# Performance work log

Hardware: AMD Instinct MI355X
Metric: run time of the kernel (lower is better)

Reference implementation:

```python
import jax, jax.numpy as jnp
import numpy as np

CANVAS = 512
SCORE_THR = 0.02
NMS_THR = 0.45
LVTOP = 1000      # cfg['lvtop'] for mm source
IMTOP = 200       # cfg['imtop']
NMS_PRE = 2000    # fixed pre-NMS candidate cap (static shape for jit)
NUM_CLASSES = 80
STRIDES = [8, 16, 32, 64, 128, 256, 512]
AR3 = [False, True, True, True, True, False, False]


def _make_priors():
    # get_scales(512): smallest=0.04, rmin=0.1, rmax=0.9, n=7
    smallest, rmin, rmax, n = 0.04, 0.1, 0.9, 7
    step = (rmax - rmin) / (n - 2)
    scales = [smallest] + [rmin + i * step for i in range(n)]
    sz = np.round(np.array(scales) * CANVAS).astype(np.int64)
    pr, lvlen = [], []
    for i, s in enumerate(STRIDES):
        fs = CANVAS // s
        ratios = [1.0, 2.0, 0.5] + ([3.0, 1.0 / 3.0] if AR3[i] else [])
        wh = [(sz[i] * np.sqrt(r), sz[i] / np.sqrt(r)) for r in ratios]
        extra = np.sqrt(float(sz[i]) * float(sz[i + 1]))  # sqrt(sz[i+1]/sz[i])*sz[i]
        wh.insert(1, (extra, extra))
        wh = np.array(wh, np.float32)            # [na, 2]
        xs = (np.arange(fs, dtype=np.float32) + 0.5) * s
        cx, cy = np.meshgrid(xs, xs)             # rows index y
        ctr = np.stack([cx, cy], -1)[:, :, None, :]  # [fs, fs, 1, 2]
        na = wh.shape[0]
        p = np.concatenate([np.broadcast_to(ctr, (fs, fs, na, 2)),
                            np.broadcast_to(wh, (fs, fs, na, 2))], -1).reshape(-1, 4)
        pr.append(p)
        lvlen.append(p.shape[0])
    return np.concatenate(pr).astype(np.float32), lvlen

PRIORS_NP, LVLEN = _make_priors()   # total 24564, lvlen=[16384,6144,1536,384,96,16,4]


def setup_inputs() -> dict:
    key = jax.random.key(0)
    k1, k2 = jax.random.split(key)
    A = PRIORS_NP.shape[0]
    cls_logits = jax.random.normal(k1, (4, A, NUM_CLASSES + 1), dtype=jnp.float32)
    reg = jax.random.normal(k2, (4, A, 4), dtype=jnp.float32)
    priors = jnp.asarray(PRIORS_NP)
    return {"cls_logits": cls_logits, "reg": reg, "priors": priors}


def _pairwise_iou(b):  # b: [K,4] xyxy
    area = (b[:, 2] - b[:, 0]) * (b[:, 3] - b[:, 1])
    lt = jnp.maximum(b[:, None, :2], b[None, :, :2])
    rb = jnp.minimum(b[:, None, 2:], b[None, :, 2:])
    wh = jnp.clip(rb - lt, 0.0)
    inter = wh[..., 0] * wh[..., 1]
    return inter / jnp.maximum(area[:, None] + area[None, :] - inter, 1e-6)


def _nms_keep(b):  # boxes sorted by descending score, class-offset applied
    m = _pairwise_iou(b) * jnp.triu(jnp.ones((NMS_PRE, NMS_PRE), b.dtype), 1)
    def body(sup, i):
        sup = sup | ((~sup[i]) & (m[i] > NMS_THR))
        return sup, None
    sup, _ = jax.lax.scan(body, jnp.zeros((NMS_PRE,), bool), jnp.arange(NMS_PRE))
    return ~sup


def reference(cls_logits, reg, priors):
    N = cls_logits.shape[0]
    C = NUM_CLASSES
    # softmax, background class is LAST (bckg_class_first=False for mm source)
    scr = jax.nn.softmax(cls_logits, axis=-1)[..., :-1]
    scr = jnp.where(scr > SCORE_THR, scr, 0.0)  # score threshold (fidx filter)
    # per-level top-k over flattened (anchor, class) pairs  [post.top_per_level]
    vals_l, anch_l, cls_l = [], [], []
    start = 0
    for lv in LVLEN:
        f = scr[:, start:start + lv, :].reshape(N, lv * C)
        k = min(LVTOP, lv * C)
        v, idx = jax.lax.top_k(f, k)
        vals_l.append(v)
        anch_l.append(start + idx // C)
        cls_l.append(idx % C)
        start += lv
    vals = jnp.concatenate(vals_l, 1)
    anch = jnp.concatenate(anch_l, 1)
    cls = jnp.concatenate(cls_l, 1)
    # fixed-size pre-NMS cap (static shapes under jit)
    v2, sel = jax.lax.top_k(vals, NMS_PRE)
    anch = jnp.take_along_axis(anch, sel, 1)
    cls = jnp.take_along_axis(cls, sel, 1)
    # decode boxes  [post.decode_boxes, mults=(0.1, 0.2), clamp=True]
    p = priors[anch]                                 # [N,K,4] cxcywh
    r = jnp.take_along_axis(reg, anch[..., None], 1)  # [N,K,4]
    cx = p[..., 0] + r[..., 0] * 0.1 * p[..., 2]
    cy = p[..., 1] + r[..., 1] * 0.1 * p[..., 3]
    w = p[..., 2] * jnp.exp(r[..., 2] * 0.2)
    h = p[..., 3] * jnp.exp(r[..., 3] * 0.2)
    boxes = jnp.stack([cx - w / 2, cy - h / 2, cx + w / 2, cy + h / 2], -1)
    boxes = jnp.clip(boxes, 0.0, float(CANVAS))
    # class-aware NMS via class offsets
    nb = boxes + cls.astype(boxes.dtype)[..., None] * (2.0 * CANVAS)
    keep = jax.vmap(_nms_keep)(nb)                   # [N,K] bool
    fs = jnp.where(keep & (v2 > 0), v2, 0.0)
    fv, fi = jax.lax.top_k(fs, IMTOP)                # imtop
    fb = jnp.take_along_axis(boxes, fi[..., None], 1)
    fc = jnp.take_along_axis(cls, fi, 1)
    fb = jnp.where(fv[..., None] > 0, fb, 0.0)
    return fb, fv, fc
```

## Files before the change

### kernel.cpp

```cpp
#include <hip/hip_runtime.h>
#include <hip/hip_bf16.h>
#include <math.h>

typedef unsigned long long u64;
typedef unsigned int u32;

#define A_TOTAL 24564
#define NCLS 80
#define NIMG 4
#define NPRE 2000
#define NLV 7
#define HBUCKETS 1024
#define BEXP_BASE 0x3CA3
#define TOTAL_G (NIMG * A_TOTAL)
#define FA 64
#define FT 256
#define NBLK_F ((TOTAL_G + FA - 1) / FA)
#define POOL_CAP_MAX 4096
#define CAPSEL 4608
#define MROWS 512
#define FTILES (MROWS / 16)

__device__ __constant__ int c_klv[NLV] = {1000,1000,1000,1000,1000,1000,320};

#define WS_HIST      0
#define WS_MCOUNT    114688
#define WS_BCOUNT    114800
#define WS_ZERO_END  114912
#define WS_PCOUNT    114912
#define WS_MAIN      121280
#define WS_BND       350656
#define WS_BOXES     1268160
#define WS_CLS       1396160
#define WS_SCORE     1428160
#define WS_MASK      1460160
#define WS_POOL      3508160

#define NZERO_W (WS_ZERO_END / 4)

__device__ inline u64 shfl_u64(u64 v, int src) {
  int lo = __shfl((int)(u32)(v & 0xFFFFFFFFULL), src);
  int hi = __shfl((int)(u32)(v >> 32), src);
  return ((u64)(u32)hi << 32) | (u32)lo;
}

__device__ inline int score_bucket(u32 bits) {
  int b = (int)(bits >> 16) - BEXP_BASE;
  return b < 0 ? 0 : (b > HBUCKETS - 1 ? HBUCKETS - 1 : b);
}

__device__ inline int level_of(int a) {
  return (a < 16384) ? 0 : (a < 22528) ? 1 : (a < 24064) ? 2 :
         (a < 24448) ? 3 : (a < 24544) ? 4 : (a < 24560) ? 5 : 6;
}

__global__ __launch_bounds__(256) void k_zero(u32* __restrict__ p) {
  int i = blockIdx.x * 256 + threadIdx.x;
  if (i < NZERO_W) p[i] = 0;
}

__device__ inline void score20(const float* __restrict__ logits, int g, int q,
                               float (&e)[20], float& rt) {
  const float* row = logits + (size_t)g * 81;
  float x[20];
#pragma unroll
  for (int i = 0; i < 20; ++i) x[i] = row[q * 20 + i];
  float x80 = (q == 3) ? row[80] : 0.f;
  float mloc = x[0];
#pragma unroll
  for (int i = 1; i < 20; ++i) mloc = fmaxf(mloc, x[i]);
  if (q == 3) mloc = fmaxf(mloc, x80);
  float m = fmaxf(mloc, __shfl_xor(mloc, 1));
  m = fmaxf(m, __shfl_xor(m, 2));
  float tq = 0.f;
#pragma unroll
  for (int i = 0; i < 20; ++i) { e[i] = expf(x[i] - m); tq += e[i]; }
  if (q == 3) tq += expf(x80 - m);
  float t = tq + __shfl_xor(tq, 1);
  t = t + __shfl_xor(t, 2);
  rt = 1.0f / t;
}

__device__ inline void wave_find_cut(const u32* __restrict__ h, int k, int lane,
                                     int& cx, int& cy) {
  u32 s = 0;
#pragma unroll
  for (int i = 0; i < 16; ++i) s += h[lane * 16 + i];
  u32 S = s;
#pragma unroll
  for (int o = 1; o < 64; o <<= 1) {
    u32 t = (u32)__shfl_down((int)S, o);
    if (lane + o < 64) S += t;
  }
  u32 total = (u32)__shfl((int)S, 0);
  if (total <= (u32)k) { cx = -1; cy = 0; return; }
  u64 bm = __ballot(S >= (u32)k);
  int L0 = 63 - (int)__clzll((long long)bm);
  u32 Sup = (u32)__shfl_down((int)S, 1);
  if (lane == 63) Sup = 0;
  int rcx = 0, rcy = 0;
  if (lane == L0) {
    u32 cum = Sup;
    for (int i = 15; i >= 0; --i) {
      u32 c = h[lane * 16 + i];
      if (cum + c >= (u32)k) { rcx = lane * 16 + i; rcy = k - (int)cum; break; }
      cum += c;
    }
  }
  cx = __shfl(rcx, L0);
  cy = __shfl(rcy, L0);
}

__global__ __launch_bounds__(FT) void k_fused(const float* __restrict__ logits,
                                              u32* __restrict__ histG,
                                              u64* __restrict__ pool,
                                              u32* __restrict__ pcount, int cap) {
  __shared__ u32 sh[HBUCKETS];
  __shared__ int nm;
  int tid = threadIdx.x, bx = blockIdx.x;
  for (int b = tid; b < HBUCKETS; b += FT) sh[b] = 0;
  if (tid == 0) nm = 0;
  int la = tid >> 2, q = tid & 3;
  int g = bx * FA + la;
  bool valid = g < TOTAL_G;
  int g0 = bx * FA;
  int seg0 = (g0 / A_TOTAL) * NLV + level_of(g0 % A_TOTAL);
  int seg = seg0, a = 0;
  float e[20];
  float rt = 0.f;
  if (valid) {
    int img = g / A_TOTAL;
    a = g - img * A_TOTAL;
    seg = img * NLV + level_of(a);
    score20(logits, g, q, e, rt);
  }
  int uniform = __syncthreads_and((int)(!valid || seg == seg0));
  if (valid) {
    u32* hdst = uniform ? sh : (histG + (size_t)seg * HBUCKETS);
    int c0 = q * 20;
    u32 wmask = 0;
#pragma unroll
    for (int i = 0; i < 20; ++i) {
      float s = e[i] * rt;
      if (s > 0.02f) wmask |= (1u << i);
    }
    int cnt = __popc(wmask);
    int basep = 0;
    if (cnt) basep = atomicAdd(&nm, cnt);
    while (wmask) {
      int i = __ffs(wmask) - 1;
      wmask &= wmask - 1;
      float s = e[i] * rt;
      u32 bits = __float_as_uint(s);
      atomicAdd(&hdst[score_bucket(bits)], 1u);
      if (basep < cap)
        pool[(size_t)bx * cap + basep] =
            ((u64)bits << 32) | (u64)(0xFFFFFFFFu - (u32)(a * NCLS + c0 + i));
      ++basep;
    }
  }
  __syncthreads();
  if (uniform) {
    u32* hseg = histG + (size_t)seg0 * HBUCKETS;
    for (int b = tid; b < HBUCKETS; b += FT) {
      u32 v = sh[b];
      if (v) atomicAdd(&hseg[b], v);
    }
  }
  if (tid == 0) pcount[bx] = (u32)nm;
}

__global__ __launch_bounds__(FT) void k_filter(const float* __restrict__ logits,
                                               const u64* __restrict__ pool,
                                               const u32* __restrict__ pcount,
                                               const u32* __restrict__ histG, int cap,
                                               u64* __restrict__ mainG, u32* __restrict__ mcount,
                                               u64* __restrict__ bndG, u32* __restrict__ bcount) {
  __shared__ int lcx4[4];
  __shared__ u64 mk[1024]; __shared__ unsigned char msg_[1024];
  __shared__ u64 bkl[256]; __shared__ unsigned char bsg[256];
  __shared__ int nm, nb, cm[4], cb[4], basem[4], baseb[4], wm[4], wb[4];
  int tid = threadIdx.x, bx = blockIdx.x;
  if (tid < 4) { cm[tid] = 0; cb[tid] = 0; wm[tid] = 0; wb[tid] = 0; }
  if (tid == 0) { nm = 0; nb = 0; }
  int g0 = bx * FA;
  int img0 = g0 / A_TOTAL;
  int alo = g0 - img0 * A_TOTAL;
  int gN = g0 + FA - 1; if (gN > TOTAL_G - 1) gN = TOTAL_G - 1;
  int seg_lo = img0 * NLV + level_of(alo);
  int seg_hi = (gN / A_TOTAL) * NLV + level_of(gN % A_TOTAL);
  int nseg = seg_hi - seg_lo + 1;
  int wid = tid >> 6, lane = tid & 63;
  if (wid < nseg) {
    int cx, cy;
    wave_find_cut(histG + (size_t)(seg_lo + wid) * HBUCKETS,
                  c_klv[(seg_lo + wid) % NLV], lane, cx, cy);
    if (lane == 0) lcx4[wid] = cx;
  }
  __syncthreads();
  int n = (int)pcount[bx];
  if (n <= cap) {
    for (int t = tid; t < n; t += FT) {
      u64 key = pool[(size_t)bx * cap + t];
      u32 bits = (u32)(key >> 32);
      u32 flat = 0xFFFFFFFFu - (u32)(key & 0xFFFFFFFFULL);
      int a = (int)(flat / NCLS);
      int img = (a >= alo) ? img0 : img0 + 1;
      int seg = img * NLV + level_of(a);
      int si = seg - seg_lo;
      int ctx = lcx4[si];
      int bk = score_bucket(bits);
      if (ctx < 0 || bk > ctx) {
        int p = atomicAdd(&nm, 1);
        if (p < 1024) { mk[p] = key; msg_[p] = (unsigned char)si; atomicAdd(&cm[si], 1); }
        else { u32 pg = atomicAdd(&mcount[seg], 1u); if (pg < 1024) mainG[(size_t)seg * 1024 + pg] = key; }
      } else if (bk == ctx) {
        int p = atomicAdd(&nb, 1);
        if (p < 256) { bkl[p] = key; bsg[p] = (unsigned char)si; atomicAdd(&cb[si], 1); }
        else { u32 pg = atomicAdd(&bcount[seg], 1u); if (pg < 4096) bndG[(size_t)seg * 4096 + pg] = key; }
      }
    }
  } else {
    int la = tid >> 2, q = tid & 3;
    int g = g0 + la;
    if (g < TOTAL_G) {
      int img = g / A_TOTAL;
      int a = g - img * A_TOTAL;
      int seg = img * NLV + level_of(a);
      int si = seg - seg_lo;
      int ctx = lcx4[si];
      float e[20];
      float rt;
      score20(logits, g, q, e, rt);
      int c0 = q * 20;
      for (int i = 0; i < 20; ++i) {
        float s = e[i] * rt;
        if (s > 0.02f) {
          u32 bits = __float_as_uint(s);
          int bk = score_bucket(bits);
          u64 key = ((u64)bits << 32) | (u64)(0xFFFFFFFFu - (u32)(a * NCLS + c0 + i));
          if (ctx < 0 || bk > ctx) {
            int p = atomicAdd(&nm, 1);
            if (p < 1024) { mk[p] = key; msg_[p] = (unsigned char)si; atomicAdd(&cm[si], 1); }
            else { u32 pg = atomicAdd(&mcount[seg], 1u); if (pg < 1024) mainG[(size_t)seg * 1024 + pg] = key; }
          } else if (bk == ctx) {
            int p = atomicAdd(&nb, 1);
            if (p < 256) { bkl[p] = key; bsg[p] = (unsigned char)si; atomicAdd(&cb[si], 1); }
            else { u32 pg = atomicAdd(&bcount[seg], 1u); if (pg < 4096) bndG[(size_t)seg * 4096 + pg] = key; }
          }
        }
      }
    }
  }
  __syncthreads();
  if (tid < nseg) {
    if (cm[tid] > 0) basem[tid] = (int)atomicAdd(&mcount[seg_lo + tid], (u32)cm[tid]);
    if (cb[tid] > 0) baseb[tid] = (int)atomicAdd(&bcount[seg_lo + tid], (u32)cb[tid]);
  }
  __syncthreads();
  int tm = nm < 1024 ? nm : 1024;
  for (int idx = tid; idx < tm; idx += FT) {
    int si = msg_[idx];
    int slot = atomicAdd(&wm[si], 1);
    int d = basem[si] + slot;
    if (d < 1024) mainG[(size_t)(seg_lo + si) * 1024 + d] = mk[idx];
  }
  int tb = nb < 256 ? nb : 256;
  for (int idx = tid; idx < tb; idx += FT) {
    int si = bsg[idx];
    int slot = atomicAdd(&wb[si], 1);
    int d = baseb[si] + slot;
    if (d < 4096) bndG[(size_t)(seg_lo + si) * 4096 + d] = bkl[idx];
  }
}

__device__ inline void bitonic_desc(u64* s, int n) {
  for (int k = 2; k <= n; k <<= 1)
    for (int j = k >> 1; j > 0; j >>= 1) {
      __syncthreads();
      for (int i = threadIdx.x; i < n; i += blockDim.x) {
        int l = i ^ j;
        if (l > i) {
          u64 a = s[i], b = s[l];
          if (((i & k) == 0) ? (a < b) : (a > b)) { s[i] = b; s[l] = a; }
        }
      }
    }
  __syncthreads();
}

__global__ __launch_bounds__(1024) void k_refine(const u32* __restrict__ histG,
                                                 const u64* __restrict__ bndG,
                                                 const u32* __restrict__ bcount,
                                                 u64* __restrict__ mainG, u32* __restrict__ mcount) {
  int seg = blockIdx.x;
  __shared__ int sh_cx, sh_cy;
  __shared__ u64 s[4096];
  int tid = threadIdx.x, lane = tid & 63;
  if (tid < 64) {
    int cx, cy;
    wave_find_cut(histG + (size_t)seg * HBUCKETS, c_klv[seg % NLV], lane, cx, cy);
    if (lane == 0) { sh_cx = cx; sh_cy = cy; }
  }
  __syncthreads();
  if (sh_cx < 0) return;
  int m = (int)bcount[seg]; if (m > 4096) m = 4096;
  int n = 64; while (n < m) n <<= 1;
  for (int t = tid; t < n; t += 1024)
    s[t] = (t < m) ? bndG[(size_t)seg * 4096 + t] : 0ULL;
  bitonic_desc(s, n);
  int kp = sh_cy; if (kp > m) kp = m;
  int base = (int)mcount[seg];
  for (int t = tid; t < kp; t += 1024) {
    int p = base + t;
    if (p < 1024) mainG[(size_t)seg * 1024 + p] = s[t];
  }
  __syncthreads();
  if (tid == 0) {
    int nb = base + kp;
    mcount[seg] = (u32)(nb > 1024 ? 1024 : nb);
  }
}

__global__ __launch_bounds__(1024) void k_gsel(const u32* __restrict__ histG,
                                               const u64* __restrict__ mainG,
                                               const u32* __restrict__ mcount,
                                               const float4* __restrict__ priors,
                                               const float4* __restrict__ reg,
                                               float4* __restrict__ boxesG,
                                               int* __restrict__ clsG,
                                               float* __restrict__ scoreG) {
  int img = blockIdx.x;
  int tid = threadIdx.x, wid = tid >> 6, lane = tid & 63;
  __shared__ u32 H[HBUCKETS];
  __shared__ u32 cntb[HBUCKETS];
  __shared__ u32 Sarr[HBUCKETS];
  __shared__ u32 cnt2[HBUCKETS];
  __shared__ u64 sel[CAPSEL];
  __shared__ int lcx[NLV], lcy[NLV];
  __shared__ int sh_gx, sh_gy, sh_cC, sh_cand, sh_sgx;
  if (tid == 0) { sh_cC = 0; sh_cand = 0; sh_sgx = -1; }
  if (wid < NLV) {
    int cx, cy;
    wave_find_cut(histG + (size_t)(img * NLV + wid) * HBUCKETS, c_klv[wid], lane, cx, cy);
    if (lane == 0) { lcx[wid] = cx; lcy[wid] = cy; }
  }
  __syncthreads();
  for (int b = tid; b < HBUCKETS; b += 1024) {
    u32 acc = 0;
#pragma unroll
    for (int l = 0; l < NLV; ++l) {
      u32 h = histG[(size_t)(img * NLV + l) * HBUCKETS + b];
      int cx = lcx[l];
      if (cx < 0 || b > cx) acc += h;
      else if (b == cx) acc += (u32)lcy[l];
    }
    H[b] = acc;
    cntb[b] = 0;
    cnt2[b] = 0;
  }
  __syncthreads();
  if (wid == 0) {
    int gx, gy;
    wave_find_cut(H, NPRE, lane, gx, gy);
    if (lane == 0) { sh_gx = gx; sh_gy = gy; }
  }
  __syncthreads();
  int gx = sh_gx, gy = sh_gy;
  int mcap[NLV];
#pragma unroll
  for (int l = 0; l < NLV; ++l) { int c = (int)mcount[img * NLV + l]; mcap[l] = c > 1024 ? 1024 : c; }
  for (int l = 0; l < NLV; ++l)
    for (int t = tid; t < mcap[l]; t += 1024) {
      u64 key = mainG[(size_t)(img * NLV + l) * 1024 + t];
      int b = score_bucket((u32)(key >> 32));
      if (gx < 0 || b > gx) atomicAdd(&cntb[b], 1u);
      else if (b == gx) atomicAdd(&sh_cC, 1);
    }
  __syncthreads();
  for (int b = tid; b < HBUCKETS; b += 1024) Sarr[b] = cntb[b];
  __syncthreads();
  {
    u32* A = Sarr; u32* B = H;
    for (int o = 1; o < HBUCKETS; o <<= 1) {
      for (int b = tid; b < HBUCKETS; b += 1024)
        B[b] = A[b] + ((b + o < HBUCKETS) ? A[b + o] : 0u);
      __syncthreads();
      u32* tmp = A; A = B; B = tmp;
    }
  }
  int cA = (int)Sarr[0];
  int cC = sh_cC;
  int cand = (gx >= 0) ? cC : 0;
  int sgx = -1;
  if (gx >= 0 && cA + cC > CAPSEL) {
    for (int b = tid; b < HBUCKETS; b += 1024) H[b] = 0;
    __syncthreads();
    for (int l = 0; l < NLV; ++l)
      for (int t = tid; t < mcap[l]; t += 1024) {
        u64 key = mainG[(size_t)(img * NLV + l) * 1024 + t];
        u32 bits = (u32)(key >> 32);
        if (score_bucket(bits) == gx) atomicAdd(&H[(bits >> 6) & 1023], 1u);
      }
    __syncthreads();
    if (wid == 0) {
      int a1, a2;
      wave_find_cut(H, gy, lane, a1, a2);
      if (lane == 0) sh_sgx = a1;
    }
    __syncthreads();
    sgx = sh_sgx;
    if (sgx >= 0) {
      for (int s2 = tid; s2 < HBUCKETS; s2 += 1024)
        if (s2 >= sgx) { u32 v = H[s2]; if (v) atomicAdd(&sh_cand, (int)v); }
      __syncthreads();
      cand = sh_cand;
    }
    if (cA + cand > CAPSEL) cand = CAPSEL - cA;
  }
  __syncthreads();
  for (int l = 0; l < NLV; ++l)
    for (int t = tid; t < mcap[l]; t += 1024) {
      u64 key = mainG[(size_t)(img * NLV + l) * 1024 + t];
      u32 bits = (u32)(key >> 32);
      int b = score_bucket(bits);
      bool inc = false; int segbase = 0, seglen = 0;
      if (gx < 0 || b > gx) {
        inc = true; segbase = (int)(Sarr[b] - cntb[b]); seglen = (int)cntb[b];
      } else if (b == gx) {
        inc = (sgx < 0) || ((int)((bits >> 6) & 1023) >= sgx);
        segbase = (int)Sarr[b]; seglen = cand;
      }
      if (inc) {
        int slot = (int)atomicAdd(&cnt2[b], 1u);
        if (slot < seglen) sel[segbase + slot] = key;
      }
    }
  __syncthreads();
  int total = cA + cand;
  u64 myk[5]; int myp[5];
#pragma unroll
  for (int it = 0; it < 5; ++it) {
    int t = tid + it * 1024;
    myp[it] = -1; myk[it] = 0;
    if (t < total) {
      u64 key = sel[t];
      u32 bits = (u32)(key >> 32);
      int b = score_bucket(bits);
      int segbase, seglen;
      if (gx >= 0 && b == gx) { segbase = (int)Sarr[b]; seglen = cand; }
      else { segbase = (int)(Sarr[b] - cntb[b]); seglen = (int)cntb[b]; }
      int r = 0;
      for (int u = 0; u < seglen; ++u) r += (sel[segbase + u] > key) ? 1 : 0;
      myk[it] = key; myp[it] = segbase + r;
    }
  }
  __syncthreads();
#pragma unroll
  for (int it = 0; it < 5; ++it) if (myp[it] >= 0) sel[myp[it]] = myk[it];
  __syncthreads();
  for (int t = tid; t < NPRE; t += 1024) {
    u64 key = (t < total) ? sel[t] : 0ULL;
    float4 bx = make_float4(0.f, 0.f, 0.f, 0.f);
    int c = -1;
    float sc = 0.f;
    if (key != 0ULL) {
      sc = __uint_as_float((u32)(key >> 32));
      u32 flat = 0xFFFFFFFFu - (u32)(key & 0xFFFFFFFFULL);
      int a = (int)(flat / NCLS);
      c = (int)(flat % NCLS);
      float4 p = priors[a];
      float4 r = reg[(size_t)img * A_TOTAL + a];
      float cx = p.x + (r.x * 0.1f) * p.z;
      float cy = p.y + (r.y * 0.1f) * p.w;
      float w = p.z * expf(r.z * 0.2f);
      float h = p.w * expf(r.w * 0.2f);
      bx.x = fminf(fmaxf(cx - w * 0.5f, 0.f), 512.f);
      bx.y = fminf(fmaxf(cy - h * 0.5f, 0.f), 512.f);
      bx.z = fminf(fmaxf(cx + w * 0.5f, 0.f), 512.f);
      bx.w = fminf(fmaxf(cy + h * 0.5f, 0.f), 512.f);
    }
    boxesG[(size_t)img * NPRE + t] = bx;
    clsG[(size_t)img * NPRE + t] = c;
    scoreG[(size_t)img * NPRE + t] = sc;
  }
}

__global__ __launch_bounds__(256) void k_mask(const float4* __restrict__ boxesG,
                                              const int* __restrict__ clsG,
                                              u64* __restrict__ maskG) {
  __shared__ float4 lb[NPRE];
  __shared__ short lc[NPRE];
  int img = blockIdx.x / (MROWS / 4);
  int rb = (blockIdx.x % (MROWS / 4)) * 4;
  for (int t = threadIdx.x; t < NPRE; t += 256) {
    lb[t] = boxesG[(size_t)img * NPRE + t];
    lc[t] = (short)clsG[(size_t)img * NPRE + t];
  }
  __syncthreads();
  int w = threadIdx.x >> 6, lane = threadIdx.x & 63;
  int i = rb + w;
  float4 bi = lb[i];
  short ci = lc[i];
  float ai = (bi.z - bi.x) * (bi.w - bi.y);
  u64* mrow = maskG + ((size_t)img * MROWS + i) * 32;
  for (int ch = 0; ch < 32; ++ch) {
    int j = ch * 64 + lane;
    bool pred = false;
    if (j < NPRE && j > i) {
      if (lc[j] == ci) {
        float4 bj = lb[j];
        float xx1 = fmaxf(bi.x, bj.x), yy1 = fmaxf(bi.y, bj.y);
        float xx2 = fminf(bi.z, bj.z), yy2 = fminf(bi.w, bj.w);
        float ww = fmaxf(xx2 - xx1, 0.f), hh = fmaxf(yy2 - yy1, 0.f);
        float inter = ww * hh;
        float aj = (bj.z - bj.x) * (bj.w - bj.y);
        float iou = inter / fmaxf(ai + aj - inter, 1e-6f);
        pred = iou > 0.45f;
      }
    }
    u64 word = __ballot(pred);
    if (lane == 0) mrow[ch] = word;
  }
}

__global__ __launch_bounds__(256) void k_scanfinal(const u64* __restrict__ maskG,
                                                   const float4* __restrict__ boxesG,
                                                   const int* __restrict__ clsG,
                                                   const float* __restrict__ scoreG,
                                                   float* __restrict__ out) {
  int img = blockIdx.x;
  int tid = threadIdx.x;
  int wid = tid >> 6, lane = tid & 63;
  __shared__ u64 sh_remv[32];
  __shared__ u64 fbm[16][32];
  __shared__ u32 keptList[216];
  __shared__ int sh_cnt, sh_done, sh_fall, sh_stop;
  __shared__ int kpref[257];
  __shared__ unsigned short S[NPRE];
  if (tid == 0) { sh_cnt = 0; sh_done = 0; sh_fall = 0; sh_stop = 0; }
  __syncthreads();
  u64 remv = 0;
  int cnt = 0;
  if (tid < 64) {
    int wl = lane & 31;
    const u64* M = maskG + (size_t)img * MROWS * 32;
    u64 cur[16], nxt[16];
#pragma unroll
    for (int r = 0; r < 16; ++r) cur[r] = M[(size_t)r * 32 + wl];
    for (int t = 0; t < FTILES; ++t) {
      if (t < FTILES - 1) {
#pragma unroll
        for (int r = 0; r < 16; ++r) nxt[r] = M[(size_t)((t + 1) * 16 + r) * 32 + wl];
      }
#pragma unroll
      for (int r = 0; r < 16; ++r) {
        int i = t * 16 + r;
        u64 rm = shfl_u64(remv, i >> 6);
        if (!((rm >> (i & 63)) & 1ULL)) {
          remv |= cur[r];
          if (lane == 0 && cnt < 216) keptList[cnt] = (u32)i;
          ++cnt;
        }
      }
#pragma unroll
      for (int r = 0; r < 16; ++r) cur[r] = nxt[r];
      if (cnt >= 200) break;
    }
    if (lane == 0) { sh_cnt = cnt < 216 ? cnt : 216; sh_fall = (cnt < 200) ? 1 : 0; }
  }
  __syncthreads();
  if (sh_fall) {
    for (int ft = FTILES; ft < 125; ++ft) {
      for (int r = wid; r < 16; r += 4) {
        int i = ft * 16 + r;
        float4 bi = boxesG[(size_t)img * NPRE + i];
        int ci = clsG[(size_t)img * NPRE + i];
        float ai = (bi.z - bi.x) * (bi.w - bi.y);
        for (int ch = 0; ch < 32; ++ch) {
          int j = ch * 64 + lane;
          bool pred = false;
          if (j < NPRE && j > i && clsG[(size_t)img * NPRE + j] == ci) {
            float4 bj = boxesG[(size_t)img * NPRE + j];
            float xx1 = fmaxf(bi.x, bj.x), yy1 = fmaxf(bi.y, bj.y);
            float xx2 = fminf(bi.z, bj.z), yy2 = fminf(bi.w, bj.w);
            float ww = fmaxf(xx2 - xx1, 0.f), hh = fmaxf(yy2 - yy1, 0.f);
            float inter = ww * hh;
            float aj = (bj.z - bj.x) * (bj.w - bj.y);
            float iou = inter / fmaxf(ai + aj - inter, 1e-6f);
            pred = iou > 0.45f;
          }
          u64 word = __ballot(pred);
          if (lane == 0) fbm[r][ch] = word;
        }
      }
      __syncthreads();
      if (tid < 64) {
        int wl = lane & 31;
#pragma unroll
        for (int r = 0; r < 16; ++r) {
          int i = ft * 16 + r;
          u64 rm = shfl_u64(remv, i >> 6);
          if (!((rm >> (i & 63)) & 1ULL)) {
            remv |= fbm[r][wl];
            if (lane == 0 && cnt < 216) keptList[cnt] = (u32)i;
            ++cnt;
          }
        }
        if (lane == 0 && (cnt >= 200 || ft == 124)) {
          sh_stop = 1;
          sh_cnt = cnt < 216 ? cnt : 216;
          if (cnt < 200) sh_done = 1;
        }
        if (ft == 124 && lane < 32) sh_remv[lane] = remv;
      }
      __syncthreads();
      if (sh_stop) break;
    }
  }
  __syncthreads();
  int nK = sh_cnt;
  if (sh_done && nK < 200) {
    int base = tid * 8;
    bool sb[8];
    int scnt = 0;
#pragma unroll
    for (int e = 0; e < 8; ++e) {
      int i = base + e;
      bool sup = (i < NPRE) && ((sh_remv[i >> 6] >> (i & 63)) & 1ULL);
      sb[e] = sup;
      scnt += sup ? 1 : 0;
    }
    kpref[tid + 1] = scnt;
    if (tid == 0) kpref[0] = 0;
    __syncthreads();
    if (tid == 0) {
      int acc = 0;
      for (int t = 1; t <= 256; ++t) { acc += kpref[t]; kpref[t] = acc; }
    }
    __syncthreads();
    int sp = kpref[tid];
#pragma unroll
    for (int e = 0; e < 8; ++e) {
      int i = base + e;
      if (i < NPRE && sb[e]) S[sp++] = (unsigned short)i;
    }
    __syncthreads();
    if (tid < 200) {
      float fv = 0.f;
      float4 fb = make_float4(0.f, 0.f, 0.f, 0.f);
      int fc;
      if (tid < nK) {
        int idx = (int)keptList[tid];
        fv = scoreG[(size_t)img * NPRE + idx];
        fb = boxesG[(size_t)img * NPRE + idx];
        fc = clsG[(size_t)img * NPRE + idx];
      } else {
        int idx = S[tid - nK];
        fc = clsG[(size_t)img * NPRE + idx];
      }
      float* fbo = out + (size_t)img * 800 + tid * 4;
      fbo[0] = fb.x; fbo[1] = fb.y; fbo[2] = fb.z; fbo[3] = fb.w;
      out[3200 + (size_t)img * 200 + tid] = fv;
      out[4000 + (size_t)img * 200 + tid] = (float)fc;
    }
  } else {
    if (tid < 200) {
      int idx = (int)keptList[tid];
      float fv = scoreG[(size_t)img * NPRE + idx];
      float4 fb = boxesG[(size_t)img * NPRE + idx];
      int fc = clsG[(size_t)img * NPRE + idx];
      float* fbo = out + (size_t)img * 800 + tid * 4;
      fbo[0] = fb.x; fbo[1] = fb.y; fbo[2] = fb.z; fbo[3] = fb.w;
      out[3200 + (size_t)img * 200 + tid] = fv;
      out[4000 + (size_t)img * 200 + tid] = (float)fc;
    }
  }
}

extern "C" void kernel_launch(void* const* d_in, const int* in_sizes, int n_in,
                              void* d_out, int out_size, void* d_ws, size_t ws_size,
                              hipStream_t stream) {
  const float* logits = (const float*)d_in[0];
  const float4* reg = (const float4*)d_in[1];
  const float4* priors = (const float4*)d_in[2];
  char* ws = (char*)d_ws;
  u32* hist = (u32*)(ws + WS_HIST);
  u32* mcount = (u32*)(ws + WS_MCOUNT);
  u32* bcount = (u32*)(ws + WS_BCOUNT);
  u32* pcount = (u32*)(ws + WS_PCOUNT);
  u64* mainL = (u64*)(ws + WS_MAIN);
  u64* bndL = (u64*)(ws + WS_BND);
  float4* boxes = (float4*)(ws + WS_BOXES);
  int* cls = (int*)(ws + WS_CLS);
  float* score = (float*)(ws + WS_SCORE);
  u64* mask = (u64*)(ws + WS_MASK);
  u64* pool = (u64*)(ws + WS_POOL);

  size_t avail = ws_size > (size_t)WS_POOL ? ws_size - (size_t)WS_POOL : 0;
  int cap = (int)(avail / ((size_t)NBLK_F * 8));
  if (cap > POOL_CAP_MAX) cap = POOL_CAP_MAX;

  k_zero<<<(NZERO_W + 255) / 256, 256, 0, stream>>>((u32*)d_ws);
  k_fused<<<NBLK_F, FT, 0, stream>>>(logits, hist, pool, pcount, cap);
  k_filter<<<NBLK_F, FT, 0, stream>>>(logits, pool, pcount, hist, cap,
                                      mainL, mcount, bndL, bcount);
  k_refine<<<28, 1024, 0, stream>>>(hist, bndL, bcount, mainL, mcount);
  k_gsel<<<NIMG, 1024, 0, stream>>>(hist, mainL, mcount, priors, reg, boxes, cls, score);
  k_mask<<<NIMG * (MROWS / 4), 256, 0, stream>>>(boxes, cls, mask);
  k_scanfinal<<<NIMG, 256, 0, stream>>>(mask, boxes, cls, score, (float*)d_out);
}
```

Before: 107.3 us.

## Fold boundary-bucket refinement into k_gsel and interleave class loads across lanes

Removes the separate k_refine kernel, which bitonic-sorted each segment's boundary-bucket keys. k_gsel now ranks each boundary key by brute-force counting against the other boundary keys and keeps those ranked below the per-level cut, doing this in the counting, sub-histogram and scatter passes. Separately, score20 now has each of the four lanes in a quad read classes q+4i, so neighbouring lanes touch neighbouring floats for better-coalesced loads. The quadratic rank count is repeated up to three times on only four blocks and could be costly if boundary buckets are large; the total is also clamped to CAPSEL.

```diff
diff --git a/kernel.cpp b/kernel.cpp
--- a/kernel.cpp
+++ b/kernel.cpp
@@ -64,7 +64,7 @@
   const float* row = logits + (size_t)g * 81;
   float x[20];
 #pragma unroll
-  for (int i = 0; i < 20; ++i) x[i] = row[q * 20 + i];
+  for (int i = 0; i < 20; ++i) x[i] = row[q + 4 * i];
   float x80 = (q == 3) ? row[80] : 0.f;
   float mloc = x[0];
 #pragma unroll
@@ -137,7 +137,6 @@
   int uniform = __syncthreads_and((int)(!valid || seg == seg0));
   if (valid) {
     u32* hdst = uniform ? sh : (histG + (size_t)seg * HBUCKETS);
-    int c0 = q * 20;
     u32 wmask = 0;
 #pragma unroll
     for (int i = 0; i < 20; ++i) {
@@ -155,7 +154,7 @@
       atomicAdd(&hdst[score_bucket(bits)], 1u);
       if (basep < cap)
         pool[(size_t)bx * cap + basep] =
-            ((u64)bits << 32) | (u64)(0xFFFFFFFFu - (u32)(a * NCLS + c0 + i));
+            ((u64)bits << 32) | (u64)(0xFFFFFFFFu - (u32)(a * NCLS + q + 4 * i));
       ++basep;
     }
   }
@@ -232,13 +231,12 @@
       float e[20];
       float rt;
       score20(logits, g, q, e, rt);
-      int c0 = q * 20;
       for (int i = 0; i < 20; ++i) {
         float s = e[i] * rt;
         if (s > 0.02f) {
           u32 bits = __float_as_uint(s);
           int bk = score_bucket(bits);
-          u64 key = ((u64)bits << 32) | (u64)(0xFFFFFFFFu - (u32)(a * NCLS + c0 + i));
+          u64 key = ((u64)bits << 32) | (u64)(0xFFFFFFFFu - (u32)(a * NCLS + q + 4 * i));
           if (ctx < 0 || bk > ctx) {
             int p = atomicAdd(&nm, 1);
             if (p < 1024) { mk[p] = key; msg_[p] = (unsigned char)si; atomicAdd(&cm[si], 1); }
@@ -274,57 +272,11 @@
   }
 }
 
-__device__ inline void bitonic_desc(u64* s, int n) {
-  for (int k = 2; k <= n; k <<= 1)
-    for (int j = k >> 1; j > 0; j >>= 1) {
-      __syncthreads();
-      for (int i = threadIdx.x; i < n; i += blockDim.x) {
-        int l = i ^ j;
-        if (l > i) {
-          u64 a = s[i], b = s[l];
-          if (((i & k) == 0) ? (a < b) : (a > b)) { s[i] = b; s[l] = a; }
-        }
-      }
-    }
-  __syncthreads();
-}
-
-__global__ __launch_bounds__(1024) void k_refine(const u32* __restrict__ histG,
-                                                 const u64* __restrict__ bndG,
-                                                 const u32* __restrict__ bcount,
-                                                 u64* __restrict__ mainG, u32* __restrict__ mcount) {
-  int seg = blockIdx.x;
-  __shared__ int sh_cx, sh_cy;
-  __shared__ u64 s[4096];
-  int tid = threadIdx.x, lane = tid & 63;
-  if (tid < 64) {
-    int cx, cy;
-    wave_find_cut(histG + (size_t)seg * HBUCKETS, c_klv[seg % NLV], lane, cx, cy);
-    if (lane == 0) { sh_cx = cx; sh_cy = cy; }
-  }
-  __syncthreads();
-  if (sh_cx < 0) return;
-  int m = (int)bcount[seg]; if (m > 4096) m = 4096;
-  int n = 64; while (n < m) n <<= 1;
-  for (int t = tid; t < n; t += 1024)
-    s[t] = (t < m) ? bndG[(size_t)seg * 4096 + t] : 0ULL;
-  bitonic_desc(s, n);
-  int kp = sh_cy; if (kp > m) kp = m;
-  int base = (int)mcount[seg];
-  for (int t = tid; t < kp; t += 1024) {
-    int p = base + t;
-    if (p < 1024) mainG[(size_t)seg * 1024 + p] = s[t];
-  }
-  __syncthreads();
-  if (tid == 0) {
-    int nb = base + kp;
-    mcount[seg] = (u32)(nb > 1024 ? 1024 : nb);
-  }
-}
-
 __global__ __launch_bounds__(1024) void k_gsel(const u32* __restrict__ histG,
                                                const u64* __restrict__ mainG,
                                                const u32* __restrict__ mcount,
+                                               const u64* __restrict__ bndG,
+                                               const u32* __restrict__ bcount,
                                                const float4* __restrict__ priors,
                                                const float4* __restrict__ reg,
                                                float4* __restrict__ boxesG,
@@ -367,9 +319,12 @@
   }
   __syncthreads();
   int gx = sh_gx, gy = sh_gy;
-  int mcap[NLV];
-#pragma unroll
-  for (int l = 0; l < NLV; ++l) { int c = (int)mcount[img * NLV + l]; mcap[l] = c > 1024 ? 1024 : c; }
+  int mcap[NLV], bcap[NLV];
+#pragma unroll
+  for (int l = 0; l < NLV; ++l) {
+    int c = (int)mcount[img * NLV + l]; mcap[l] = c > 1024 ? 1024 : c;
+    int bc = (lcx[l] >= 0) ? (int)bcount[img * NLV + l] : 0; bcap[l] = bc > 4096 ? 4096 : bc;
+  }
   for (int l = 0; l < NLV; ++l)
     for (int t = tid; t < mcap[l]; t += 1024) {
       u64 key = mainG[(size_t)(img * NLV + l) * 1024 + t];
@@ -377,6 +332,19 @@
       if (gx < 0 || b > gx) atomicAdd(&cntb[b], 1u);
       else if (b == gx) atomicAdd(&sh_cC, 1);
     }
+  for (int l = 0; l < NLV; ++l) {
+    const u64* B = bndG + (size_t)(img * NLV + l) * 4096;
+    for (int t = tid; t < bcap[l]; t += 1024) {
+      u64 key = B[t];
+      int r = 0;
+      for (int u = 0; u < bcap[l]; ++u) r += (B[u] > key) ? 1 : 0;
+      if (r < lcy[l]) {
+        int b = lcx[l];
+        if (gx < 0 || b > gx) atomicAdd(&cntb[b], 1u);
+        else if (b == gx) atomicAdd(&sh_cC, 1);
+      }
+    }
+  }
   __syncthreads();
   for (int b = tid; b < HBUCKETS; b += 1024) Sarr[b] = cntb[b];
   __syncthreads();
@@ -402,6 +370,16 @@
         u32 bits = (u32)(key >> 32);
         if (score_bucket(bits) == gx) atomicAdd(&H[(bits >> 6) & 1023], 1u);
       }
+    for (int l = 0; l < NLV; ++l) {
+      if (lcx[l] != gx) continue;
+      const u64* B = bndG + (size_t)(img * NLV + l) * 4096;
+      for (int t = tid; t < bcap[l]; t += 1024) {
+        u64 key = B[t];
+        int r = 0;
+        for (int u = 0; u < bcap[l]; ++u) r += (B[u] > key) ? 1 : 0;
+        if (r < lcy[l]) atomicAdd(&H[((u32)(key >> 32) >> 6) & 1023], 1u);
+      }
+    }
     __syncthreads();
     if (wid == 0) {
       int a1, a2;
@@ -436,8 +414,31 @@
         if (slot < seglen) sel[segbase + slot] = key;
       }
     }
+  for (int l = 0; l < NLV; ++l) {
+    const u64* B = bndG + (size_t)(img * NLV + l) * 4096;
+    for (int t = tid; t < bcap[l]; t += 1024) {
+      u64 key = B[t];
+      int r = 0;
+      for (int u = 0; u < bcap[l]; ++u) r += (B[u] > key) ? 1 : 0;
+      if (r >= lcy[l]) continue;
+      u32 bits = (u32)(key >> 32);
+      int b = lcx[l];
+      bool inc = false; int segbase = 0, seglen = 0;
+      if (gx < 0 || b > gx) {
+        inc = true; segbase = (int)(Sarr[b] - cntb[b]); seglen = (int)cntb[b];
+      } else if (b == gx) {
+        inc = (sgx < 0) || ((int)((bits >> 6) & 1023) >= sgx);
+        segbase = (int)Sarr[b]; seglen = cand;
+      }
+      if (inc) {
+        int slot = (int)atomicAdd(&cnt2[b], 1u);
+        if (slot < seglen) sel[segbase + slot] = key;
+      }
+    }
+  }
   __syncthreads();
   int total = cA + cand;
+  if (total > CAPSEL) total = CAPSEL;
   u64 myk[5]; int myp[5];
 #pragma unroll
   for (int it = 0; it < 5; ++it) {
@@ -705,8 +706,8 @@
   k_fused<<<NBLK_F, FT, 0, stream>>>(logits, hist, pool, pcount, cap);
   k_filter<<<NBLK_F, FT, 0, stream>>>(logits, pool, pcount, hist, cap,
                                       mainL, mcount, bndL, bcount);
-  k_refine<<<28, 1024, 0, stream>>>(hist, bndL, bcount, mainL, mcount);
-  k_gsel<<<NIMG, 1024, 0, stream>>>(hist, mainL, mcount, priors, reg, boxes, cls, score);
+  k_gsel<<<NIMG, 1024, 0, stream>>>(hist, mainL, mcount, bndL, bcount,
+                                    priors, reg, boxes, cls, score);
   k_mask<<<NIMG * (MROWS / 4), 256, 0, stream>>>(boxes, cls, mask);
   k_scanfinal<<<NIMG, 256, 0, stream>>>(mask, boxes, cls, score, (float*)d_out);
 }
```

Measured after the change: 109.2 us. No clear change (+1.8%).
